# Kernel optimization log

Hardware: AMD Instinct MI355X
Metric: run time of the kernel (lower is better)

Reference implementation:

```python
import jax, jax.numpy as jnp
import numpy as np

N, E, F_IN, HID, HEADS, OUT = 50000, 800000, 128, 64, 4, 40


def gat_layer(x, src, dst, n, W, a_src, a_dst, b, heads, ch):
    # PyG GATConv: h = x @ W per head; e_ij = LeakyReLU(a_src.h_j + a_dst.h_i)
    h = (x @ W).reshape(n, heads, ch)
    al_s = jnp.einsum('nhc,hc->nh', h, a_src)  # source-side logit term
    al_d = jnp.einsum('nhc,hc->nh', h, a_dst)  # target-side logit term
    e = jax.nn.leaky_relu(al_s[src] + al_d[dst], negative_slope=0.2)  # [E,H]
    m = jax.ops.segment_max(e, dst, num_segments=n)  # stable softmax per target node
    e = jnp.exp(e - m[dst])
    s = jax.ops.segment_sum(e, dst, num_segments=n)
    alpha = e / s[dst]  # [E,H]
    out = jax.ops.segment_sum(h[src] * alpha[:, :, None], dst, num_segments=n)  # [n,H,C]
    return out.reshape(n, heads * ch) + b


def gat_forward(x, src, dst, W0, as0, ad0, b0, W1, as1, ad1, b1, W2, as2, ad2, b2):
    n = x.shape[0]
    x = jax.nn.elu(gat_layer(x, src, dst, n, W0, as0, ad0, b0, HEADS, HID))
    x = jax.nn.elu(gat_layer(x, src, dst, n, W1, as1, ad1, b1, HEADS, HID))
    x = gat_layer(x, src, dst, n, W2, as2, ad2, b2, 1, OUT)
    return jax.nn.log_softmax(x, axis=1)


def setup_inputs() -> dict:
    key = jax.random.key(0)
    ks = jax.random.split(key, 16)
    x = jax.random.normal(ks[0], (N, F_IN), dtype=jnp.float32)
    edge_index = jax.random.randint(ks[1], (2, E), 0, N, dtype=jnp.int64)
    g = lambda k, sh: jax.random.normal(k, sh, dtype=jnp.float32) * (1.0 / np.sqrt(sh[0]))
    d_hid = HID * HEADS
    return {
        'x': x, 'edge_index': edge_index,
        'W0': g(ks[2], (F_IN, d_hid)), 'as0': g(ks[3], (HEADS, HID)), 'ad0': g(ks[4], (HEADS, HID)), 'b0': jnp.zeros((d_hid,), jnp.float32),
        'W1': g(ks[5], (d_hid, d_hid)), 'as1': g(ks[6], (HEADS, HID)), 'ad1': g(ks[7], (HEADS, HID)), 'b1': jnp.zeros((d_hid,), jnp.float32),
        'W2': g(ks[8], (d_hid, OUT)), 'as2': g(ks[9], (1, OUT)), 'ad2': g(ks[10], (1, OUT)), 'b2': jnp.zeros((OUT,), jnp.float32),
    }


def reference(x, edge_index, W0, as0, ad0, b0, W1, as1, ad1, b1, W2, as2, ad2, b2):
    n = x.shape[0]
    loops = jnp.arange(n, dtype=edge_index.dtype)  # PyG add_self_loops=True
    src = jnp.concatenate([edge_index[0], loops])
    dst = jnp.concatenate([edge_index[1], loops])
    return gat_forward(x, src, dst, W0, as0, ad0, b0, W1, as1, ad1, b1, W2, as2, ad2, b2)
```

## Files before the change

### kernel.cpp

```cpp
#include <hip/hip_runtime.h>
#include <hip/hip_fp16.h>
#include <math.h>

#define NODES 50000
#define NEDGES 800000
#define TOT_E (NEDGES + NODES)
#define SCAN_B 256
#define SCAN_NB ((NODES + SCAN_B - 1) / SCAN_B)

typedef __attribute__((ext_vector_type(8))) _Float16 half8v;
typedef __attribute__((ext_vector_type(4))) float f32x4;

union U2H { uint u; __half2 h; };

static __device__ __forceinline__ float lrelu(float z) {
  return z > 0.f ? z : 0.2f * z;
}
static __device__ __forceinline__ ushort f2h(float f) {
  __half h = __float2half_rn(f);
  return *reinterpret_cast<ushort*>(&h);
}
static __device__ __forceinline__ void wave_lds_fence() {
  __builtin_amdgcn_wave_barrier();
  asm volatile("s_waitcnt lgkmcnt(0)" ::: "memory");
  __builtin_amdgcn_sched_barrier(0);
}

__global__ void k_hist(const int* __restrict__ dst, int* __restrict__ counts) {
  int stride = gridDim.x * blockDim.x;
  for (int i = blockIdx.x * blockDim.x + threadIdx.x; i < TOT_E; i += stride) {
    int d = (i < NEDGES) ? dst[i] : (i - NEDGES);
    atomicAdd(&counts[d], 1);
  }
}

__global__ __launch_bounds__(SCAN_B) void k_scan_red(const int* __restrict__ counts,
                                                     int* __restrict__ bsum) {
  __shared__ int sm[SCAN_B];
  int idx = blockIdx.x * SCAN_B + threadIdx.x;
  int v = (idx < NODES) ? counts[idx] : 0;
  sm[threadIdx.x] = v;
  __syncthreads();
  for (int off = SCAN_B / 2; off > 0; off >>= 1) {
    if (threadIdx.x < off) sm[threadIdx.x] += sm[threadIdx.x + off];
    __syncthreads();
  }
  if (threadIdx.x == 0) bsum[blockIdx.x] = sm[0];
}

__global__ __launch_bounds__(256) void k_scan_part(const int* __restrict__ bsum,
                                                   int* __restrict__ bpre) {
  __shared__ int sm[256];
  int tid = threadIdx.x;
  int v = (tid < SCAN_NB) ? bsum[tid] : 0;
  sm[tid] = v;
  __syncthreads();
  for (int off = 1; off < 256; off <<= 1) {
    int t = (tid >= off) ? sm[tid - off] : 0;
    __syncthreads();
    sm[tid] += t;
    __syncthreads();
  }
  if (tid < SCAN_NB) bpre[tid] = sm[tid] - v;
}

__global__ __launch_bounds__(SCAN_B) void k_scan_emit(const int* __restrict__ counts,
    const int* __restrict__ bpre, int* __restrict__ offs, int* __restrict__ cur) {
  __shared__ int sm[SCAN_B];
  int idx = blockIdx.x * SCAN_B + threadIdx.x;
  int tid = threadIdx.x;
  int v = (idx < NODES) ? counts[idx] : 0;
  sm[tid] = v;
  __syncthreads();
  for (int off = 1; off < SCAN_B; off <<= 1) {
    int t = (tid >= off) ? sm[tid - off] : 0;
    __syncthreads();
    sm[tid] += t;
    __syncthreads();
  }
  int base = bpre[blockIdx.x];
  int excl = base + sm[tid] - v;
  if (idx < NODES) { offs[idx] = excl; cur[idx] = excl; }
  if (idx == NODES - 1) offs[NODES] = excl + v;
}

__global__ void k_scatter(const int* __restrict__ src, const int* __restrict__ dst,
                          int* __restrict__ cur, int* __restrict__ ssrc) {
  int stride = gridDim.x * blockDim.x;
  for (int i = blockIdx.x * blockDim.x + threadIdx.x; i < TOT_E; i += stride) {
    int s, d;
    if (i < NEDGES) { s = src[i]; d = dst[i]; } else { s = i - NEDGES; d = s; }
    int pos = atomicAdd(&cur[d], 1);
    ssrc[pos] = s;
  }
}

__global__ void k_cast4(const float* __restrict__ X, ushort* __restrict__ Xh, int total4) {
  int stride = gridDim.x * blockDim.x;
  for (int i = blockIdx.x * blockDim.x + threadIdx.x; i < total4; i += stride) {
    float4 v = *(const float4*)&X[i * 4];
    ushort4 o;
    o.x = f2h(v.x); o.y = f2h(v.y); o.z = f2h(v.z); o.w = f2h(v.w);
    *(ushort4*)&Xh[i * 4] = o;
  }
}

__global__ void k_packB(const float* __restrict__ W, ushort* __restrict__ Bp,
                        int N, int NF, int total) {
  int idx = blockIdx.x * blockDim.x + threadIdx.x;
  if (idx >= total) return;
  int i = idx & 7;
  int lane = (idx >> 3) & 63;
  int rem = idx >> 9;
  int nf = rem % NF;
  int kf = rem / NF;
  int k = kf * 32 + (lane >> 4) * 8 + i;
  int col = nf * 16 + (lane & 15);
  float v = (col < N) ? W[(size_t)k * N + col] : 0.f;
  Bp[idx] = f2h(v);
}

template<int KF, int NFW, int CG, int HEADS, int NF_TOT>
__global__ __launch_bounds__(256, 2) void k_gemm_reg(
    const ushort* __restrict__ A, const ushort* __restrict__ Bp,
    ushort* __restrict__ H, const float* __restrict__ a_s, const float* __restrict__ a_d,
    float* __restrict__ al_s, float* __restrict__ al_d, int M, int N, int K) {
  int wib = threadIdx.x >> 6;
  int lane = threadIdx.x & 63;
  int lg = lane >> 4;
  int lr = lane & 15;
  int cg, strip0, sstride;
  if (CG == 4) { cg = wib; strip0 = blockIdx.x; sstride = gridDim.x; }
  else { cg = 0; strip0 = blockIdx.x * 4 + wib; sstride = gridDim.x * 4; }

  half8v b[KF][NFW];
#pragma unroll
  for (int kf = 0; kf < KF; ++kf)
#pragma unroll
    for (int n = 0; n < NFW; ++n)
      b[kf][n] = *(const half8v*)(Bp + ((size_t)(kf * NF_TOT + cg * NFW + n) * 64 + lane) * 8);

  float asc[NFW], adc[NFW];
#pragma unroll
  for (int n = 0; n < NFW; ++n) {
    int col = (cg * NFW + n) * 16 + lr;
    bool ok = col < N;
    asc[n] = ok ? a_s[col] : 0.f;
    adc[n] = ok ? a_d[col] : 0.f;
  }

  int nstrips = M >> 4;
  for (int strip = strip0; strip < nstrips; strip += sstride) {
    const ushort* arow = A + (size_t)(strip * 16 + lr) * K + lg * 8;
    half8v a[KF];
#pragma unroll
    for (int kf = 0; kf < KF; ++kf) a[kf] = *(const half8v*)(arow + kf * 32);
    f32x4 acc[NFW];
#pragma unroll
    for (int n = 0; n < NFW; ++n) acc[n] = (f32x4){0.f, 0.f, 0.f, 0.f};
#pragma unroll
    for (int kf = 0; kf < KF; ++kf)
#pragma unroll
      for (int n = 0; n < NFW; ++n)
        acc[n] = __builtin_amdgcn_mfma_f32_16x16x32_f16(a[kf], b[kf][n], acc[n], 0, 0, 0);

#pragma unroll
    for (int n = 0; n < NFW; ++n) {
      int col = (cg * NFW + n) * 16 + lr;
      if (col < N) {
#pragma unroll
        for (int r = 0; r < 4; ++r) {
          int row = strip * 16 + lg * 4 + r;
          H[(size_t)row * N + col] = f2h(acc[n][r]);
        }
      }
    }

    float ps[4], pd[4];
#pragma unroll
    for (int r = 0; r < 4; ++r) {
      float s = 0.f, d = 0.f;
#pragma unroll
      for (int n = 0; n < NFW; ++n) {
        s += acc[n][r] * asc[n];
        d += acc[n][r] * adc[n];
      }
      ps[r] = s; pd[r] = d;
    }
#pragma unroll
    for (int off = 1; off <= 8; off <<= 1)
#pragma unroll
      for (int t = 0; t < 4; ++t) {
        ps[t] += __shfl_xor(ps[t], off);
        pd[t] += __shfl_xor(pd[t], off);
      }
    if (lr < 4) {
      int row = strip * 16 + lg * 4 + lr;
      if (HEADS == 4) {
        al_s[row * 4 + cg] = ps[lr];
        al_d[row * 4 + cg] = pd[lr];
      } else {
        al_s[row] = ps[lr];
        al_d[row] = pd[lr];
      }
    }
  }
}

__global__ __launch_bounds__(256) void k_agg4(const ushort* __restrict__ hb,
    const float* __restrict__ al_s, const float* __restrict__ al_d,
    const int* __restrict__ offs, const int* __restrict__ ssrc,
    const float* __restrict__ bias, ushort* __restrict__ outb) {
  __shared__ uint4 s_pack[4][64][2];
  int w = threadIdx.x >> 6;
  int wid = (blockIdx.x * blockDim.x + threadIdx.x) >> 6;
  if (wid >= NODES) return;
  int lane = threadIdx.x & 63;
  int beg = offs[wid], end = offs[wid + 1];
  float4 ald4 = *(const float4*)&al_d[wid * 4];

  float m[4] = {-1e30f, -1e30f, -1e30f, -1e30f};
  for (int i = beg + lane; i < end; i += 64) {
    int sv = ssrc[i];
    float4 a4 = *(const float4*)&al_s[sv * 4];
    m[0] = fmaxf(m[0], lrelu(a4.x + ald4.x));
    m[1] = fmaxf(m[1], lrelu(a4.y + ald4.y));
    m[2] = fmaxf(m[2], lrelu(a4.z + ald4.z));
    m[3] = fmaxf(m[3], lrelu(a4.w + ald4.w));
  }
#pragma unroll
  for (int off = 1; off <= 32; off <<= 1) {
#pragma unroll
    for (int h = 0; h < 4; ++h) m[h] = fmaxf(m[h], __shfl_xor(m[h], off));
  }

  int half = lane >> 5;
  int cl = lane & 31;
  int hh = cl >> 3;
  uint clb = (uint)cl * 8;
  float sacc[4] = {0.f, 0.f, 0.f, 0.f};
  __half2 z2 = __float2half2_rn(0.f);
  __half2 acc2a[4] = {z2, z2, z2, z2};
  __half2 acc2b[4] = {z2, z2, z2, z2};

  for (int cb = beg; cb < end; cb += 64) {
    int cnt = min(64, end - cb);
    wave_lds_fence();
    if (lane < cnt) {
      uint sv = (uint)ssrc[cb + lane];
      float4 a4 = *(const float4*)&al_s[sv * 4];
      float t0 = __expf(lrelu(a4.x + ald4.x) - m[0]);
      float t1 = __expf(lrelu(a4.y + ald4.y) - m[1]);
      float t2 = __expf(lrelu(a4.z + ald4.z) - m[2]);
      float t3 = __expf(lrelu(a4.w + ald4.w) - m[3]);
      sacc[0] += t0; sacc[1] += t1; sacc[2] += t2; sacc[3] += t3;
      U2H p0, p1, p2, p3;
      p0.h = __float2half2_rn(t0); p1.h = __float2half2_rn(t1);
      p2.h = __float2half2_rn(t2); p3.h = __float2half2_rn(t3);
      s_pack[w][lane][0] = make_uint4(sv, p0.u, sv, p1.u);
      s_pack[w][lane][1] = make_uint4(sv, p2.u, sv, p3.u);
    }
    wave_lds_fence();
    int e = half;
    for (; e + 2 < cnt; e += 4) {
      const uint2* pk0 = (const uint2*)&s_pack[w][e][0];
      const uint2* pk1 = (const uint2*)&s_pack[w][e + 2][0];
      uint2 k0 = pk0[hh], k1 = pk1[hh];
      U2H a0, a1; a0.u = k0.y; a1.u = k1.y;
      uint4 hv0 = *(const uint4*)(hb + ((k0.x << 8) + clb));
      uint4 hv1 = *(const uint4*)(hb + ((k1.x << 8) + clb));
      U2H v;
      v.u = hv0.x; acc2a[0] = __hfma2(a0.h, v.h, acc2a[0]);
      v.u = hv0.y; acc2a[1] = __hfma2(a0.h, v.h, acc2a[1]);
      v.u = hv0.z; acc2a[2] = __hfma2(a0.h, v.h, acc2a[2]);
      v.u = hv0.w; acc2a[3] = __hfma2(a0.h, v.h, acc2a[3]);
      v.u = hv1.x; acc2b[0] = __hfma2(a1.h, v.h, acc2b[0]);
      v.u = hv1.y; acc2b[1] = __hfma2(a1.h, v.h, acc2b[1]);
      v.u = hv1.z; acc2b[2] = __hfma2(a1.h, v.h, acc2b[2]);
      v.u = hv1.w; acc2b[3] = __hfma2(a1.h, v.h, acc2b[3]);
    }
    for (; e < cnt; e += 2) {
      const uint2* pk = (const uint2*)&s_pack[w][e][0];
      uint2 k0 = pk[hh];
      U2H a0; a0.u = k0.y;
      uint4 hv = *(const uint4*)(hb + ((k0.x << 8) + clb));
      U2H v;
      v.u = hv.x; acc2a[0] = __hfma2(a0.h, v.h, acc2a[0]);
      v.u = hv.y; acc2a[1] = __hfma2(a0.h, v.h, acc2a[1]);
      v.u = hv.z; acc2a[2] = __hfma2(a0.h, v.h, acc2a[2]);
      v.u = hv.w; acc2a[3] = __hfma2(a0.h, v.h, acc2a[3]);
    }
  }
#pragma unroll
  for (int off = 1; off <= 32; off <<= 1) {
#pragma unroll
    for (int h = 0; h < 4; ++h) sacc[h] += __shfl_xor(sacc[h], off);
  }
  float invs = 1.f / sacc[hh];
  ushort4 ores[2];
#pragma unroll
  for (int j = 0; j < 4; ++j) {
    U2H t; t.h = __hadd2(acc2a[j], acc2b[j]);
    U2H o; o.u = __shfl_xor(t.u, 32);
    t.h = __hadd2(t.h, o.h);
    float lo = __low2float(t.h) * invs + bias[cl * 8 + j * 2];
    float hi = __high2float(t.h) * invs + bias[cl * 8 + j * 2 + 1];
    lo = lo > 0.f ? lo : __expf(lo) - 1.f;
    hi = hi > 0.f ? hi : __expf(hi) - 1.f;
    ((ushort*)ores)[j * 2]     = f2h(lo);
    ((ushort*)ores)[j * 2 + 1] = f2h(hi);
  }
  if (half == 0) {
    *(ushort4*)(outb + (size_t)wid * 256 + cl * 8)     = ores[0];
    *(ushort4*)(outb + (size_t)wid * 256 + cl * 8 + 4) = ores[1];
  }
}

__global__ __launch_bounds__(256) void k_agg1(const ushort* __restrict__ hb,
    const float* __restrict__ al_s, const float* __restrict__ al_d,
    const int* __restrict__ offs, const int* __restrict__ ssrc,
    const float* __restrict__ bias, float* __restrict__ out) {
  __shared__ uint2 s_pack[4][64];
  int w = threadIdx.x >> 6;
  int wid = (blockIdx.x * blockDim.x + threadIdx.x) >> 6;
  if (wid >= NODES) return;
  int lane = threadIdx.x & 63;
  int beg = offs[wid], end = offs[wid + 1];
  float ald = al_d[wid];

  float m = -1e30f;
  for (int i = beg + lane; i < end; i += 64)
    m = fmaxf(m, lrelu(al_s[ssrc[i]] + ald));
#pragma unroll
  for (int off = 1; off <= 32; off <<= 1) m = fmaxf(m, __shfl_xor(m, off));

  int q = lane >> 4;
  int cq = lane & 15;
  bool act = cq < 10;
  uint cqb = (uint)cq * 4;
  float sacc = 0.f;
  __half2 z2 = __float2half2_rn(0.f);
  __half2 acc2a[2] = {z2, z2};
  __half2 acc2b[2] = {z2, z2};
  for (int cb = beg; cb < end; cb += 64) {
    int cnt = min(64, end - cb);
    wave_lds_fence();
    if (lane < cnt) {
      uint sv = (uint)ssrc[cb + lane];
      float t = __expf(lrelu(al_s[sv] + ald) - m);
      sacc += t;
      U2H p; p.h = __float2half2_rn(t);
      s_pack[w][lane] = make_uint2(sv, p.u);
    }
    wave_lds_fence();
    int e = q;
    for (; e + 4 < cnt; e += 8) {
      uint2 k0 = s_pack[w][e], k1 = s_pack[w][e + 4];
      U2H a0, a1; a0.u = k0.y; a1.u = k1.y;
      if (act) {
        uint2 hv0 = *(const uint2*)(hb + (k0.x * 40u + cqb));
        uint2 hv1 = *(const uint2*)(hb + (k1.x * 40u + cqb));
        U2H v;
        v.u = hv0.x; acc2a[0] = __hfma2(a0.h, v.h, acc2a[0]);
        v.u = hv0.y; acc2a[1] = __hfma2(a0.h, v.h, acc2a[1]);
        v.u = hv1.x; acc2b[0] = __hfma2(a1.h, v.h, acc2b[0]);
        v.u = hv1.y; acc2b[1] = __hfma2(a1.h, v.h, acc2b[1]);
      }
    }
    for (; e < cnt; e += 4) {
      uint2 k0 = s_pack[w][e];
      U2H a0; a0.u = k0.y;
      if (act) {
        uint2 hv = *(const uint2*)(hb + (k0.x * 40u + cqb));
        U2H v;
        v.u = hv.x; acc2a[0] = __hfma2(a0.h, v.h, acc2a[0]);
        v.u = hv.y; acc2a[1] = __hfma2(a0.h, v.h, acc2a[1]);
      }
    }
  }
#pragma unroll
  for (int off = 1; off <= 32; off <<= 1) sacc += __shfl_xor(sacc, off);
  float invs = 1.f / sacc;
  float vv[4];
#pragma unroll
  for (int j = 0; j < 2; ++j) {
    U2H t; t.h = __hadd2(acc2a[j], acc2b[j]);
    U2H o;
    o.u = __shfl_xor(t.u, 16); t.h = __hadd2(t.h, o.h);
    o.u = __shfl_xor(t.u, 32); t.h = __hadd2(t.h, o.h);
    vv[j * 2]     = __low2float(t.h) * invs;
    vv[j * 2 + 1] = __high2float(t.h) * invs;
  }
  float mm = -1e30f;
  if (act) {
#pragma unroll
    for (int j = 0; j < 4; ++j) {
      vv[j] += bias[cq * 4 + j];
      mm = fmaxf(mm, vv[j]);
    }
  }
#pragma unroll
  for (int off = 1; off <= 8; off <<= 1) mm = fmaxf(mm, __shfl_xor(mm, off));
  float se = 0.f;
  if (act) {
#pragma unroll
    for (int j = 0; j < 4; ++j) se += __expf(vv[j] - mm);
  }
#pragma unroll
  for (int off = 1; off <= 8; off <<= 1) se += __shfl_xor(se, off);
  if (act && q == 0) {
    float lse = mm + __logf(se);
    float4 o;
    o.x = vv[0] - lse; o.y = vv[1] - lse; o.z = vv[2] - lse; o.w = vv[3] - lse;
    *(float4*)&out[(size_t)wid * 40 + cq * 4] = o;
  }
}

extern "C" void kernel_launch(void* const* d_in, const int* in_sizes, int n_in,
                              void* d_out, int out_size, void* d_ws, size_t ws_size,
                              hipStream_t stream) {
  const float* x   = (const float*)d_in[0];
  const int*   ei  = (const int*)d_in[1];
  const float* W0  = (const float*)d_in[2];
  const float* as0 = (const float*)d_in[3];
  const float* ad0 = (const float*)d_in[4];
  const float* b0  = (const float*)d_in[5];
  const float* W1  = (const float*)d_in[6];
  const float* as1 = (const float*)d_in[7];
  const float* ad1 = (const float*)d_in[8];
  const float* b1  = (const float*)d_in[9];
  const float* W2  = (const float*)d_in[10];
  const float* as2 = (const float*)d_in[11];
  const float* ad2 = (const float*)d_in[12];
  const float* b2  = (const float*)d_in[13];
  float* out = (float*)d_out;

  char* p = (char*)d_ws;
  auto take = [&](size_t bytes) {
    char* q = p;
    p += (bytes + 255) & ~(size_t)255;
    return (void*)q;
  };
  ushort* xb0 = (ushort*)take((size_t)NODES * 128 * 2);
  ushort* xb1 = (ushort*)take((size_t)NODES * 256 * 2);
  ushort* xb2 = (ushort*)take((size_t)NODES * 256 * 2);
  ushort* hb  = (ushort*)take((size_t)NODES * 256 * 2);
  float* als  = (float*)take((size_t)NODES * 4 * 4);
  float* ald  = (float*)take((size_t)NODES * 4 * 4);
  int* ssrc   = (int*)take((size_t)TOT_E * 4);
  int* offs   = (int*)take((size_t)(NODES + 1) * 4);
  int* cur    = (int*)take((size_t)NODES * 4);
  int* cnt    = (int*)take((size_t)NODES * 4);
  int* bsum   = (int*)take((size_t)SCAN_NB * 4);
  int* bpre   = (int*)take((size_t)SCAN_NB * 4);
  ushort* Bp0 = (ushort*)take((size_t)4 * 16 * 512 * 2);
  ushort* Bp1 = (ushort*)take((size_t)8 * 16 * 512 * 2);
  ushort* Bp2 = (ushort*)take((size_t)8 * 3 * 512 * 2);

  hipMemsetAsync(cnt, 0, (size_t)NODES * 4, stream);
  k_hist<<<2048, 256, 0, stream>>>(ei + NEDGES, cnt);
  k_scan_red<<<SCAN_NB, SCAN_B, 0, stream>>>(cnt, bsum);
  k_scan_part<<<1, 256, 0, stream>>>(bsum, bpre);
  k_scan_emit<<<SCAN_NB, SCAN_B, 0, stream>>>(cnt, bpre, offs, cur);
  k_scatter<<<2048, 256, 0, stream>>>(ei, ei + NEDGES, cur, ssrc);

  k_cast4<<<2048, 256, 0, stream>>>(x, xb0, NODES * 128 / 4);
  {
    int t0 = 4 * 16 * 512;  k_packB<<<(t0 + 255) / 256, 256, 0, stream>>>(W0, Bp0, 256, 16, t0);
    int t1 = 8 * 16 * 512;  k_packB<<<(t1 + 255) / 256, 256, 0, stream>>>(W1, Bp1, 256, 16, t1);
    int t2 = 8 * 3 * 512;   k_packB<<<(t2 + 255) / 256, 256, 0, stream>>>(W2, Bp2, 40, 3, t2);
  }

  int nwb = (NODES * 64 + 255) / 256;

  k_gemm_reg<4, 4, 4, 4, 16><<<512, 256, 0, stream>>>(xb0, Bp0, hb, as0, ad0, als, ald, NODES, 256, 128);
  k_agg4<<<nwb, 256, 0, stream>>>(hb, als, ald, offs, ssrc, b0, xb1);

  k_gemm_reg<8, 4, 4, 4, 16><<<512, 256, 0, stream>>>(xb1, Bp1, hb, as1, ad1, als, ald, NODES, 256, 256);
  k_agg4<<<nwb, 256, 0, stream>>>(hb, als, ald, offs, ssrc, b1, xb2);

  k_gemm_reg<8, 3, 1, 1, 3><<<512, 256, 0, stream>>>(xb2, Bp2, hb, as2, ad2, als, ald, NODES, 40, 256);
  k_agg1<<<nwb, 256, 0, stream>>>(hb, als, ald, offs, ssrc, b2, out);
}
```

Before: 334.5 us.

## Map aggregation nodes to half-waves and fuse setup kernels into one launch

New measurement: 304.3 us. -9.0%, faster.

```diff
diff --git a/kernel.cpp b/kernel.cpp
--- a/kernel.cpp
+++ b/kernel.cpp
@@ -26,11 +26,48 @@
   __builtin_amdgcn_sched_barrier(0);
 }
 
-__global__ void k_hist(const int* __restrict__ dst, int* __restrict__ counts) {
-  int stride = gridDim.x * blockDim.x;
-  for (int i = blockIdx.x * blockDim.x + threadIdx.x; i < TOT_E; i += stride) {
-    int d = (i < NEDGES) ? dst[i] : (i - NEDGES);
-    atomicAdd(&counts[d], 1);
+static __device__ __forceinline__ void packB_one(const float* __restrict__ W,
+    ushort* __restrict__ Bp, int N, int NF, int idx) {
+  int i = idx & 7;
+  int lane = (idx >> 3) & 63;
+  int rem = idx >> 9;
+  int nf = rem % NF;
+  int kf = rem / NF;
+  int k = kf * 32 + (lane >> 4) * 8 + i;
+  int col = nf * 16 + (lane & 15);
+  float v = (col < N) ? W[(size_t)k * N + col] : 0.f;
+  Bp[idx] = f2h(v);
+}
+
+__global__ __launch_bounds__(256) void k_setup(const int* __restrict__ dst,
+    int* __restrict__ counts, const float* __restrict__ x, ushort* __restrict__ xb0,
+    const float* __restrict__ W0, ushort* __restrict__ Bp0,
+    const float* __restrict__ W1, ushort* __restrict__ Bp1,
+    const float* __restrict__ W2, ushort* __restrict__ Bp2) {
+  int gb = blockIdx.x;
+  int tid = threadIdx.x;
+  if (gb < 2048) {
+    int stride = 2048 * 256;
+    for (int i = gb * 256 + tid; i < TOT_E; i += stride) {
+      int d = (i < NEDGES) ? dst[i] : (i - NEDGES);
+      atomicAdd(&counts[d], 1);
+    }
+  } else if (gb < 4048) {
+    int total4 = NODES * 128 / 4;
+    int stride = 2000 * 256;
+    for (int i = (gb - 2048) * 256 + tid; i < total4; i += stride) {
+      float4 v = *(const float4*)&x[i * 4];
+      ushort4 o;
+      o.x = f2h(v.x); o.y = f2h(v.y); o.z = f2h(v.z); o.w = f2h(v.w);
+      *(ushort4*)&xb0[i * 4] = o;
+    }
+  } else {
+    int b = gb - 4048;
+    int stride = 48 * 256;
+    int base = b * 256 + tid;
+    for (int idx = base; idx < 4 * 16 * 512; idx += stride) packB_one(W0, Bp0, 256, 16, idx);
+    for (int idx = base; idx < 8 * 16 * 512; idx += stride) packB_one(W1, Bp1, 256, 16, idx);
+    for (int idx = base; idx < 8 * 3 * 512; idx += stride)  packB_one(W2, Bp2, 40, 3, idx);
   }
 }
 
@@ -95,31 +132,6 @@
   }
 }
 
-__global__ void k_cast4(const float* __restrict__ X, ushort* __restrict__ Xh, int total4) {
-  int stride = gridDim.x * blockDim.x;
-  for (int i = blockIdx.x * blockDim.x + threadIdx.x; i < total4; i += stride) {
-    float4 v = *(const float4*)&X[i * 4];
-    ushort4 o;
-    o.x = f2h(v.x); o.y = f2h(v.y); o.z = f2h(v.z); o.w = f2h(v.w);
-    *(ushort4*)&Xh[i * 4] = o;
-  }
-}
-
-__global__ void k_packB(const float* __restrict__ W, ushort* __restrict__ Bp,
-                        int N, int NF, int total) {
-  int idx = blockIdx.x * blockDim.x + threadIdx.x;
-  if (idx >= total) return;
-  int i = idx & 7;
-  int lane = (idx >> 3) & 63;
-  int rem = idx >> 9;
-  int nf = rem % NF;
-  int kf = rem / NF;
-  int k = kf * 32 + (lane >> 4) * 8 + i;
-  int col = nf * 16 + (lane & 15);
-  float v = (col < N) ? W[(size_t)k * N + col] : 0.f;
-  Bp[idx] = f2h(v);
-}
-
 template<int KF, int NFW, int CG, int HEADS, int NF_TOT>
 __global__ __launch_bounds__(256, 2) void k_gemm_reg(
     const ushort* __restrict__ A, const ushort* __restrict__ Bp,
@@ -211,16 +223,17 @@
     const float* __restrict__ al_s, const float* __restrict__ al_d,
     const int* __restrict__ offs, const int* __restrict__ ssrc,
     const float* __restrict__ bias, ushort* __restrict__ outb) {
-  __shared__ uint4 s_pack[4][64][2];
-  int w = threadIdx.x >> 6;
-  int wid = (blockIdx.x * blockDim.x + threadIdx.x) >> 6;
-  if (wid >= NODES) return;
-  int lane = threadIdx.x & 63;
-  int beg = offs[wid], end = offs[wid + 1];
-  float4 ald4 = *(const float4*)&al_d[wid * 4];
+  __shared__ uint s_sv[8][32];
+  __shared__ uint s_al[8][4][33];
+  int hw = threadIdx.x >> 5;
+  int node = (blockIdx.x * 256 + threadIdx.x) >> 5;
+  if (node >= NODES) return;
+  int l = threadIdx.x & 31;
+  int beg = offs[node], end = offs[node + 1];
+  float4 ald4 = *(const float4*)&al_d[node * 4];
 
   float m[4] = {-1e30f, -1e30f, -1e30f, -1e30f};
-  for (int i = beg + lane; i < end; i += 64) {
+  for (int i = beg + l; i < end; i += 32) {
     int sv = ssrc[i];
     float4 a4 = *(const float4*)&al_s[sv * 4];
     m[0] = fmaxf(m[0], lrelu(a4.x + ald4.x));
@@ -229,25 +242,23 @@
     m[3] = fmaxf(m[3], lrelu(a4.w + ald4.w));
   }
 #pragma unroll
-  for (int off = 1; off <= 32; off <<= 1) {
+  for (int off = 1; off <= 16; off <<= 1) {
 #pragma unroll
     for (int h = 0; h < 4; ++h) m[h] = fmaxf(m[h], __shfl_xor(m[h], off));
   }
 
-  int half = lane >> 5;
-  int cl = lane & 31;
-  int hh = cl >> 3;
-  uint clb = (uint)cl * 8;
+  int hh = l >> 3;
+  uint clb = (uint)l * 8;
   float sacc[4] = {0.f, 0.f, 0.f, 0.f};
   __half2 z2 = __float2half2_rn(0.f);
-  __half2 acc2a[4] = {z2, z2, z2, z2};
-  __half2 acc2b[4] = {z2, z2, z2, z2};
-
-  for (int cb = beg; cb < end; cb += 64) {
-    int cnt = min(64, end - cb);
+  __half2 accA[4] = {z2, z2, z2, z2};
+  __half2 accB[4] = {z2, z2, z2, z2};
+
+  for (int cb = beg; cb < end; cb += 32) {
+    int cnt = min(32, end - cb);
     wave_lds_fence();
-    if (lane < cnt) {
-      uint sv = (uint)ssrc[cb + lane];
+    if (l < cnt) {
+      uint sv = (uint)ssrc[cb + l];
       float4 a4 = *(const float4*)&al_s[sv * 4];
       float t0 = __expf(lrelu(a4.x + ald4.x) - m[0]);
       float t1 = __expf(lrelu(a4.y + ald4.y) - m[1]);
@@ -257,42 +268,53 @@
       U2H p0, p1, p2, p3;
       p0.h = __float2half2_rn(t0); p1.h = __float2half2_rn(t1);
       p2.h = __float2half2_rn(t2); p3.h = __float2half2_rn(t3);
-      s_pack[w][lane][0] = make_uint4(sv, p0.u, sv, p1.u);
-      s_pack[w][lane][1] = make_uint4(sv, p2.u, sv, p3.u);
+      s_sv[hw][l] = sv;
+      s_al[hw][0][l] = p0.u; s_al[hw][1][l] = p1.u;
+      s_al[hw][2][l] = p2.u; s_al[hw][3][l] = p3.u;
     }
     wave_lds_fence();
-    int e = half;
-    for (; e + 2 < cnt; e += 4) {
-      const uint2* pk0 = (const uint2*)&s_pack[w][e][0];
-      const uint2* pk1 = (const uint2*)&s_pack[w][e + 2][0];
-      uint2 k0 = pk0[hh], k1 = pk1[hh];
-      U2H a0, a1; a0.u = k0.y; a1.u = k1.y;
-      uint4 hv0 = *(const uint4*)(hb + ((k0.x << 8) + clb));
-      uint4 hv1 = *(const uint4*)(hb + ((k1.x << 8) + clb));
+    int e = 0;
+    for (; e + 3 < cnt; e += 4) {
+      uint sv0 = s_sv[hw][e],     sv1 = s_sv[hw][e + 1];
+      uint sv2 = s_sv[hw][e + 2], sv3 = s_sv[hw][e + 3];
+      U2H a0, a1, a2, a3;
+      a0.u = s_al[hw][hh][e];     a1.u = s_al[hw][hh][e + 1];
+      a2.u = s_al[hw][hh][e + 2]; a3.u = s_al[hw][hh][e + 3];
+      uint4 hv0 = *(const uint4*)(hb + ((sv0 << 8) + clb));
+      uint4 hv1 = *(const uint4*)(hb + ((sv1 << 8) + clb));
+      uint4 hv2 = *(const uint4*)(hb + ((sv2 << 8) + clb));
+      uint4 hv3 = *(const uint4*)(hb + ((sv3 << 8) + clb));
       U2H v;
-      v.u = hv0.x; acc2a[0] = __hfma2(a0.h, v.h, acc2a[0]);
-      v.u = hv0.y; acc2a[1] = __hfma2(a0.h, v.h, acc2a[1]);
-      v.u = hv0.z; acc2a[2] = __hfma2(a0.h, v.h, acc2a[2]);
-      v.u = hv0.w; acc2a[3] = __hfma2(a0.h, v.h, acc2a[3]);
-      v.u = hv1.x; acc2b[0] = __hfma2(a1.h, v.h, acc2b[0]);
-      v.u = hv1.y; acc2b[1] = __hfma2(a1.h, v.h, acc2b[1]);
-      v.u = hv1.z; acc2b[2] = __hfma2(a1.h, v.h, acc2b[2]);
-      v.u = hv1.w; acc2b[3] = __hfma2(a1.h, v.h, acc2b[3]);
-    }
-    for (; e < cnt; e += 2) {
-      const uint2* pk = (const uint2*)&s_pack[w][e][0];
-      uint2 k0 = pk[hh];
-      U2H a0; a0.u = k0.y;
-      uint4 hv = *(const uint4*)(hb + ((k0.x << 8) + clb));
+      v.u = hv0.x; accA[0] = __hfma2(a0.h, v.h, accA[0]);
+      v.u = hv0.y; accA[1] = __hfma2(a0.h, v.h, accA[1]);
+      v.u = hv0.z; accA[2] = __hfma2(a0.h, v.h, accA[2]);
+      v.u = hv0.w; accA[3] = __hfma2(a0.h, v.h, accA[3]);
+      v.u = hv1.x; accB[0] = __hfma2(a1.h, v.h, accB[0]);
+      v.u = hv1.y; accB[1] = __hfma2(a1.h, v.h, accB[1]);
+      v.u = hv1.z; accB[2] = __hfma2(a1.h, v.h, accB[2]);
+      v.u = hv1.w; accB[3] = __hfma2(a1.h, v.h, accB[3]);
+      v.u = hv2.x; accA[0] = __hfma2(a2.h, v.h, accA[0]);
+      v.u = hv2.y; accA[1] = __hfma2(a2.h, v.h, accA[1]);
+      v.u = hv2.z; accA[2] = __hfma2(a2.h, v.h, accA[2]);
+      v.u = hv2.w; accA[3] = __hfma2(a2.h, v.h, accA[3]);
+      v.u = hv3.x; accB[0] = __hfma2(a3.h, v.h, accB[0]);
+      v.u = hv3.y; accB[1] = __hfma2(a3.h, v.h, accB[1]);
+      v.u = hv3.z; accB[2] = __hfma2(a3.h, v.h, accB[2]);
+      v.u = hv3.w; accB[3] = __hfma2(a3.h, v.h, accB[3]);
+    }
+    for (; e < cnt; ++e) {
+      uint sv = s_sv[hw][e];
+      U2H a0; a0.u = s_al[hw][hh][e];
+      uint4 hv = *(const uint4*)(hb + ((sv << 8) + clb));
       U2H v;
-      v.u = hv.x; acc2a[0] = __hfma2(a0.h, v.h, acc2a[0]);
-      v.u = hv.y; acc2a[1] = __hfma2(a0.h, v.h, acc2a[1]);
-      v.u = hv.z; acc2a[2] = __hfma2(a0.h, v.h, acc2a[2]);
-      v.u = hv.w; acc2a[3] = __hfma2(a0.h, v.h, acc2a[3]);
-    }
-  }
-#pragma unroll
-  for (int off = 1; off <= 32; off <<= 1) {
+      v.u = hv.x; accA[0] = __hfma2(a0.h, v.h, accA[0]);
+      v.u = hv.y; accA[1] = __hfma2(a0.h, v.h, accA[1]);
+      v.u = hv.z; accA[2] = __hfma2(a0.h, v.h, accA[2]);
+      v.u = hv.w; accA[3] = __hfma2(a0.h, v.h, accA[3]);
+    }
+  }
+#pragma unroll
+  for (int off = 1; off <= 16; off <<= 1) {
 #pragma unroll
     for (int h = 0; h < 4; ++h) sacc[h] += __shfl_xor(sacc[h], off);
   }
@@ -300,94 +322,100 @@
   ushort4 ores[2];
 #pragma unroll
   for (int j = 0; j < 4; ++j) {
-    U2H t; t.h = __hadd2(acc2a[j], acc2b[j]);
-    U2H o; o.u = __shfl_xor(t.u, 32);
-    t.h = __hadd2(t.h, o.h);
-    float lo = __low2float(t.h) * invs + bias[cl * 8 + j * 2];
-    float hi = __high2float(t.h) * invs + bias[cl * 8 + j * 2 + 1];
+    U2H t; t.h = __hadd2(accA[j], accB[j]);
+    float lo = __low2float(t.h) * invs + bias[l * 8 + j * 2];
+    float hi = __high2float(t.h) * invs + bias[l * 8 + j * 2 + 1];
     lo = lo > 0.f ? lo : __expf(lo) - 1.f;
     hi = hi > 0.f ? hi : __expf(hi) - 1.f;
     ((ushort*)ores)[j * 2]     = f2h(lo);
     ((ushort*)ores)[j * 2 + 1] = f2h(hi);
   }
-  if (half == 0) {
-    *(ushort4*)(outb + (size_t)wid * 256 + cl * 8)     = ores[0];
-    *(ushort4*)(outb + (size_t)wid * 256 + cl * 8 + 4) = ores[1];
-  }
+  *(ushort4*)(outb + (size_t)node * 256 + l * 8)     = ores[0];
+  *(ushort4*)(outb + (size_t)node * 256 + l * 8 + 4) = ores[1];
 }
 
 __global__ __launch_bounds__(256) void k_agg1(const ushort* __restrict__ hb,
     const float* __restrict__ al_s, const float* __restrict__ al_d,
     const int* __restrict__ offs, const int* __restrict__ ssrc,
     const float* __restrict__ bias, float* __restrict__ out) {
-  __shared__ uint2 s_pack[4][64];
-  int w = threadIdx.x >> 6;
-  int wid = (blockIdx.x * blockDim.x + threadIdx.x) >> 6;
-  if (wid >= NODES) return;
-  int lane = threadIdx.x & 63;
-  int beg = offs[wid], end = offs[wid + 1];
-  float ald = al_d[wid];
+  __shared__ uint s_sv[8][32];
+  __shared__ uint s_al[8][32];
+  int hw = threadIdx.x >> 5;
+  int node = (blockIdx.x * 256 + threadIdx.x) >> 5;
+  if (node >= NODES) return;
+  int l = threadIdx.x & 31;
+  int beg = offs[node], end = offs[node + 1];
+  float ald = al_d[node];
 
   float m = -1e30f;
-  for (int i = beg + lane; i < end; i += 64)
+  for (int i = beg + l; i < end; i += 32)
     m = fmaxf(m, lrelu(al_s[ssrc[i]] + ald));
 #pragma unroll
-  for (int off = 1; off <= 32; off <<= 1) m = fmaxf(m, __shfl_xor(m, off));
-
-  int q = lane >> 4;
-  int cq = lane & 15;
+  for (int off = 1; off <= 16; off <<= 1) m = fmaxf(m, __shfl_xor(m, off));
+
+  int p = l >> 4;
+  int cq = l & 15;
   bool act = cq < 10;
   uint cqb = (uint)cq * 4;
   float sacc = 0.f;
   __half2 z2 = __float2half2_rn(0.f);
-  __half2 acc2a[2] = {z2, z2};
-  __half2 acc2b[2] = {z2, z2};
-  for (int cb = beg; cb < end; cb += 64) {
-    int cnt = min(64, end - cb);
+  __half2 accA[2] = {z2, z2};
+  __half2 accB[2] = {z2, z2};
+  for (int cb = beg; cb < end; cb += 32) {
+    int cnt = min(32, end - cb);
     wave_lds_fence();
-    if (lane < cnt) {
-      uint sv = (uint)ssrc[cb + lane];
+    if (l < cnt) {
+      uint sv = (uint)ssrc[cb + l];
       float t = __expf(lrelu(al_s[sv] + ald) - m);
       sacc += t;
-      U2H p; p.h = __float2half2_rn(t);
-      s_pack[w][lane] = make_uint2(sv, p.u);
+      U2H pk; pk.h = __float2half2_rn(t);
+      s_sv[hw][l] = sv;
+      s_al[hw][l] = pk.u;
     }
     wave_lds_fence();
-    int e = q;
-    for (; e + 4 < cnt; e += 8) {
-      uint2 k0 = s_pack[w][e], k1 = s_pack[w][e + 4];
-      U2H a0, a1; a0.u = k0.y; a1.u = k1.y;
+    int e = p;
+    for (; e + 6 < cnt; e += 8) {
+      uint sv0 = s_sv[hw][e],     sv1 = s_sv[hw][e + 2];
+      uint sv2 = s_sv[hw][e + 4], sv3 = s_sv[hw][e + 6];
+      U2H a0, a1, a2, a3;
+      a0.u = s_al[hw][e];     a1.u = s_al[hw][e + 2];
+      a2.u = s_al[hw][e + 4]; a3.u = s_al[hw][e + 6];
       if (act) {
-        uint2 hv0 = *(const uint2*)(hb + (k0.x * 40u + cqb));
-        uint2 hv1 = *(const uint2*)(hb + (k1.x * 40u + cqb));
+        uint2 hv0 = *(const uint2*)(hb + (sv0 * 40u + cqb));
+        uint2 hv1 = *(const uint2*)(hb + (sv1 * 40u + cqb));
+        uint2 hv2 = *(const uint2*)(hb + (sv2 * 40u + cqb));
+        uint2 hv3 = *(const uint2*)(hb + (sv3 * 40u + cqb));
         U2H v;
-        v.u = hv0.x; acc2a[0] = __hfma2(a0.h, v.h, acc2a[0]);
-        v.u = hv0.y; acc2a[1] = __hfma2(a0.h, v.h, acc2a[1]);
-        v.u = hv1.x; acc2b[0] = __hfma2(a1.h, v.h, acc2b[0]);
-        v.u = hv1.y; acc2b[1] = __hfma2(a1.h, v.h, acc2b[1]);
+        v.u = hv0.x; accA[0] = __hfma2(a0.h, v.h, accA[0]);
+        v.u = hv0.y; accA[1] = __hfma2(a0.h, v.h, accA[1]);
+        v.u = hv1.x; accB[0] = __hfma2(a1.h, v.h, accB[0]);
+        v.u = hv1.y; accB[1] = __hfma2(a1.h, v.h, accB[1]);
+        v.u = hv2.x; accA[0] = __hfma2(a2.h, v.h, accA[0]);
+        v.u = hv2.y; accA[1] = __hfma2(a2.h, v.h, accA[1]);
+        v.u = hv3.x; accB[0] = __hfma2(a3.h, v.h, accB[0]);
+        v.u = hv3.y; accB[1] = __hfma2(a3.h, v.h, accB[1]);
       }
     }
-    for (; e < cnt; e += 4) {
-      uint2 k0 = s_pack[w][e];
-      U2H a0; a0.u = k0.y;
+    for (; e < cnt; e += 2) {
+      uint sv = s_sv[hw][e];
+      U2H a0; a0.u = s_al[hw][e];
       if (act) {
-        uint2 hv = *(const uint2*)(hb + (k0.x * 40u + cqb));
+        uint2 hv = *(const uint2*)(hb + (sv * 40u + cqb));
         U2H v;
-        v.u = hv.x; acc2a[0] = __hfma2(a0.h, v.h, acc2a[0]);
-        v.u = hv.y; acc2a[1] = __hfma2(a0.h, v.h, acc2a[1]);
+        v.u = hv.x; accA[0] = __hfma2(a0.h, v.h, accA[0]);
+        v.u = hv.y; accA[1] = __hfma2(a0.h, v.h, accA[1]);
       }
     }
   }
 #pragma unroll
-  for (int off = 1; off <= 32; off <<= 1) sacc += __shfl_xor(sacc, off);
+  for (int off = 1; off <= 16; off <<= 1) sacc += __shfl_xor(sacc, off);
   float invs = 1.f / sacc;
   float vv[4];
 #pragma unroll
   for (int j = 0; j < 2; ++j) {
-    U2H t; t.h = __hadd2(acc2a[j], acc2b[j]);
-    U2H o;
-    o.u = __shfl_xor(t.u, 16); t.h = __hadd2(t.h, o.h);
-    o.u = __shfl_xor(t.u, 32); t.h = __hadd2(t.h, o.h);
+    U2H t; t.h = __hadd2(accA[j], accB[j]);
+    U2H o; o.u = __shfl_xor(t.u, 16);
+    t.h = __hadd2(t.h, o.h);
     vv[j * 2]     = __low2float(t.h) * invs;
     vv[j * 2 + 1] = __high2float(t.h) * invs;
   }
@@ -408,11 +436,11 @@
   }
 #pragma unroll
   for (int off = 1; off <= 8; off <<= 1) se += __shfl_xor(se, off);
-  if (act && q == 0) {
+  if (act && p == 0) {
     float lse = mm + __logf(se);
     float4 o;
     o.x = vv[0] - lse; o.y = vv[1] - lse; o.z = vv[2] - lse; o.w = vv[3] - lse;
-    *(float4*)&out[(size_t)wid * 40 + cq * 4] = o;
+    *(float4*)&out[(size_t)node * 40 + cq * 4] = o;
   }
 }
 
@@ -458,27 +486,20 @@
   ushort* Bp2 = (ushort*)take((size_t)8 * 3 * 512 * 2);
 
   hipMemsetAsync(cnt, 0, (size_t)NODES * 4, stream);
-  k_hist<<<2048, 256, 0, stream>>>(ei + NEDGES, cnt);
+  k_setup<<<4096, 256, 0, stream>>>(ei + NEDGES, cnt, x, xb0, W0, Bp0, W1, Bp1, W2, Bp2);
   k_scan_red<<<SCAN_NB, SCAN_B, 0, stream>>>(cnt, bsum);
   k_scan_part<<<1, 256, 0, stream>>>(bsum, bpre);
   k_scan_emit<<<SCAN_NB, SCAN_B, 0, stream>>>(cnt, bpre, offs, cur);
   k_scatter<<<2048, 256, 0, stream>>>(ei, ei + NEDGES, cur, ssrc);
 
-  k_cast4<<<2048, 256, 0, stream>>>(x, xb0, NODES * 128 / 4);
-  {
-    int t0 = 4 * 16 * 512;  k_packB<<<(t0 + 255) / 256, 256, 0, stream>>>(W0, Bp0, 256, 16, t0);
-    int t1 = 8 * 16 * 512;  k_packB<<<(t1 + 255) / 256, 256, 0, stream>>>(W1, Bp1, 256, 16, t1);
-    int t2 = 8 * 3 * 512;   k_packB<<<(t2 + 255) / 256, 256, 0, stream>>>(W2, Bp2, 40, 3, t2);
-  }
-
-  int nwb = (NODES * 64 + 255) / 256;
+  int nab = (NODES * 32 + 255) / 256;
 
   k_gemm_reg<4, 4, 4, 4, 16><<<512, 256, 0, stream>>>(xb0, Bp0, hb, as0, ad0, als, ald, NODES, 256, 128);
-  k_agg4<<<nwb, 256, 0, stream>>>(hb, als, ald, offs, ssrc, b0, xb1);
+  k_agg4<<<nab, 256, 0, stream>>>(hb, als, ald, offs, ssrc, b0, xb1);
 
   k_gemm_reg<8, 4, 4, 4, 16><<<512, 256, 0, stream>>>(xb1, Bp1, hb, as1, ad1, als, ald, NODES, 256, 256);
-  k_agg4<<<nwb, 256, 0, stream>>>(hb, als, ald, offs, ssrc, b1, xb2);
+  k_agg4<<<nab, 256, 0, stream>>>(hb, als, ald, offs, ssrc, b1, xb2);
 
   k_gemm_reg<8, 3, 1, 1, 3><<<512, 256, 0, stream>>>(xb2, Bp2, hb, as2, ad2, als, ald, NODES, 40, 256);
-  k_agg1<<<nwb, 256, 0, stream>>>(hb, als, ald, offs, ssrc, b2, out);
-}
+  k_agg1<<<nab, 256, 0, stream>>>(hb, als, ald, offs, ssrc, b2, out);
+}
```
